# Performance work log

Measured on AMD Instinct MI355X. Metric: run time of the kernel, lower is better.

The kernel has to match this reference:

```python
import jax, jax.numpy as jnp
import numpy as np

B, L, H, E, D = 4, 2048, 8, 64, 64  # seq S == L (causal mask requires square scores)


def setup_inputs() -> dict:
    key = jax.random.key(0)
    k0, k1, k2, k3, k4 = jax.random.split(key, 5)
    queries = jax.random.normal(k0, (B, L, H, E), jnp.float32)
    keys = jax.random.normal(k1, (B, L, H, E), jnp.float32)
    values = jax.random.normal(k2, (B, L, H, D), jnp.float32)
    # per-sample learned de-stationary scale (positive) and bias
    tau = jax.random.uniform(k3, (B, 1, 1), jnp.float32, 0.5, 1.5)
    delta = jax.random.normal(k4, (B, 1, L), jnp.float32) * 0.1
    return {"queries": queries, "keys": keys, "values": values, "tau": tau, "delta": delta}


def reference(queries, keys, values, tau, delta):
    Bq, Lq, Hq, Eq = queries.shape
    S = keys.shape[1]
    scale = 1.0 / jnp.sqrt(jnp.asarray(Eq, jnp.float32))
    # torch path: rearrange('b s h d l -> (b d) s h l') with s=h=d=1 -> [B,1,1,1] / [B,1,1,S]
    tau_b = tau.reshape(Bq, 1, 1, 1)
    delta_b = delta.reshape(Bq, 1, 1, -1)[..., :S]
    # scores: [B, H, L, S]
    scores = jnp.einsum('blhe,bshe->bhls', queries, keys) * tau_b + delta_b
    causal = jnp.triu(jnp.ones((Lq, S), bool), k=1)  # True above diagonal -> masked
    scores = jnp.where(causal, -jnp.inf, scores)
    A = jax.nn.softmax(scale * scores, axis=-1)  # dropout is identity in eval/reference
    V = jnp.einsum('bhls,bshd->blhd', A, values)  # [B, L, H, D]
    return V
```

## Files before the change

kernel.cpp:

```cpp
#include <hip/hip_runtime.h>
#include <hip/hip_bf16.h>

#define Bsz 4
#define Lsz 2048
#define Hsz 8

typedef __attribute__((ext_vector_type(8)))  short bf16x8;
typedef __attribute__((ext_vector_type(4)))  short bf16x4;
typedef __attribute__((ext_vector_type(4)))  float f32x4;

__device__ __forceinline__ short f2bs(float f) {
    union { float f; unsigned u; } v; v.f = f;
    unsigned r = v.u + 0x7FFFu + ((v.u >> 16) & 1u);
    return (short)(r >> 16);
}
__device__ __forceinline__ short f2bs_rh(float f) {
    return (short)((__float_as_uint(f) + 0x8000u) >> 16);
}

__device__ __forceinline__ void stage16(const short* g, short* l) {
    __builtin_amdgcn_global_load_lds(
        (const __attribute__((address_space(1))) unsigned int*)g,
        (__attribute__((address_space(3))) unsigned int*)l,
        16, 0, 0);
}

__global__ __launch_bounds__(256) void prep_kv(
    const float* __restrict__ ksrc, const float* __restrict__ vsrc,
    const float* __restrict__ delta,
    short* __restrict__ Kf, short* __restrict__ Vf, float* __restrict__ Df)
{
    const int raw = blockIdx.x;
    const int tid = threadIdx.x;
    if (raw >= 2*Bsz*Hsz*32) {
        const float c2 = 0.125f * 1.44269504f;
        const int base = ((raw - 2*Bsz*Hsz*32)*256 + tid) * 16;
        #pragma unroll
        for (int u = 0; u < 4; ++u) {
            float4 v = *(const float4*)(delta + base + u*4);
            v.x*=c2; v.y*=c2; v.z*=c2; v.w*=c2;
            *(float4*)(Df + base + u*4) = v;
        }
        return;
    }
    __shared__ float Tl[64][65];
    const bool isK = raw < Bsz*Hsz*32;
    const int bid = isK ? raw : raw - Bsz*Hsz*32;
    const int tl = bid & 31, bh = bid >> 5;
    const int b = bh >> 3, h = bh & 7;

    const int row = tid >> 2, c0 = (tid & 3) * 16;
    const float* src = (isK ? ksrc : vsrc)
                     + (((size_t)b*Lsz + tl*64 + row)*Hsz + h)*64 + c0;
    *(float4*)&Tl[row][c0]      = *(const float4*)(src);
    *(float4*)&Tl[row][c0 + 4]  = *(const float4*)(src + 4);
    *(float4*)&Tl[row][c0 + 8]  = *(const float4*)(src + 8);
    *(float4*)&Tl[row][c0 + 12] = *(const float4*)(src + 12);
    __syncthreads();

    const int lane = tid & 63, ln = lane & 15, quad = lane >> 4;
    if (isK) {
        short* dst = Kf + (size_t)bid * 4096;
        #pragma unroll
        for (int cc = 0; cc < 2; ++cc) {
            const int c  = (tid >> 6)*2 + cc;
            const int kq = c >> 1, eb = c & 1;
            const float* rp = &Tl[kq*16 + ln][eb*32 + quad*8];
            bf16x8 o = {f2bs(rp[0]),f2bs(rp[1]),f2bs(rp[2]),f2bs(rp[3]),
                        f2bs(rp[4]),f2bs(rp[5]),f2bs(rp[6]),f2bs(rp[7])};
            *(bf16x8*)(dst + c*512 + lane*8) = o;
        }
    } else {
        short* dst = Vf + (size_t)bid * 4096;
        #pragma unroll
        for (int cc = 0; cc < 2; ++cc) {
            const int c   = (tid >> 6)*2 + cc;
            const int kq  = c >> 1, dgp = c & 1;
            const int s0  = kq*16 + quad*4;
            const int d0  = dgp*32 + ln;
            const int d1  = dgp*32 + 16 + ln;
            bf16x8 o = {f2bs(Tl[s0+0][d0]), f2bs(Tl[s0+1][d0]),
                        f2bs(Tl[s0+2][d0]), f2bs(Tl[s0+3][d0]),
                        f2bs(Tl[s0+0][d1]), f2bs(Tl[s0+1][d1]),
                        f2bs(Tl[s0+2][d1]), f2bs(Tl[s0+3][d1])};
            *(bf16x8*)(dst + c*512 + lane*8) = o;
        }
    }
}

__global__ __launch_bounds__(256, 4) void dsattn_main(
    const float* __restrict__ q,
    const short* __restrict__ Kf,
    const short* __restrict__ Vf,
    const float* __restrict__ Df,
    const float* __restrict__ tau,
    float* __restrict__ out)
{
    __shared__ __align__(16) short Kb[2][4096];
    __shared__ __align__(16) short Vb[2][4096];
    __shared__ __align__(16) short Qs[4096];

    const int tid  = threadIdx.x;
    const int kq   = tid >> 6;
    const int lane = tid & 63;
    const int ln   = lane & 15;
    const int quad = lane >> 4;

    const int bh = blockIdx.x;
    const int b  = bh >> 3, h = bh & 7;
    const int y = blockIdx.y, g8 = y >> 3, a = y & 7;
    const int qt = (g8 == 0) ? 31 - 2*a : (g8 == 1) ? 2*a
                 : (g8 == 2) ? 30 - 2*a : 2*a + 1;
    const int q0 = qt * 64;
    const int T  = qt + 1;

    const float st2 = (0.125f * 1.44269504f) * tau[b];

    const short* gK = Kf + (size_t)bh*(32*4096) + kq*1024 + lane*8;
    const short* gV = Vf + (size_t)bh*(32*4096) + kq*1024 + lane*8;
    const float* Dfp = Df + (size_t)b*Lsz + kq*16 + quad*4;

    short* const myK0 = &Kb[0][kq*1024];
    short* const myV0 = &Vb[0][kq*1024];

#define STAGE(buf) do {                                                     \
        short* k_ = (buf) ? myK0 + 4096 : myK0;                             \
        short* v_ = (buf) ? myV0 + 4096 : myV0;                             \
        stage16(gK + 0*512, k_ + 0*512);                                    \
        stage16(gK + 1*512, k_ + 1*512);                                    \
        stage16(gV + 0*512, v_ + 0*512);                                    \
        stage16(gV + 1*512, v_ + 1*512);                                    \
        gK += 4096; gV += 4096;                                             \
        __builtin_amdgcn_sched_barrier(0);                                  \
    } while (0)
#define WAITN(n) do {                                                       \
        asm volatile("s_waitcnt vmcnt(" #n ")" ::: "memory");               \
        __builtin_amdgcn_sched_barrier(0);                                  \
    } while (0)

    STAGE(0);
    f32x4 dlv_c = *(const f32x4*)(Dfp); Dfp += 64;

    {
        const float* qrow = q + (((size_t)b*Lsz + q0 + kq*16 + ln)*Hsz + h)*64;
        float4 a0 = *(const float4*)(qrow + quad*8);
        float4 a1 = *(const float4*)(qrow + quad*8 + 4);
        float4 b0 = *(const float4*)(qrow + 32 + quad*8);
        float4 b1 = *(const float4*)(qrow + 32 + quad*8 + 4);
        bf16x8 q0f = {f2bs(a0.x),f2bs(a0.y),f2bs(a0.z),f2bs(a0.w),
                      f2bs(a1.x),f2bs(a1.y),f2bs(a1.z),f2bs(a1.w)};
        bf16x8 q1f = {f2bs(b0.x),f2bs(b0.y),f2bs(b0.z),f2bs(b0.w),
                      f2bs(b1.x),f2bs(b1.y),f2bs(b1.z),f2bs(b1.w)};
        *(bf16x8*)(&Qs[(kq*2+0)*512 + lane*8]) = q0f;
        *(bf16x8*)(&Qs[(kq*2+1)*512 + lane*8]) = q1f;
    }

    f32x4 oacc[4][4];
    #pragma unroll
    for (int dg = 0; dg < 4; ++dg)
        #pragma unroll
        for (int qg = 0; qg < 4; ++qg)
            oacc[dg][qg] = (f32x4){0.f,0.f,0.f,0.f};
    float l_acc[4] = {0.f,0.f,0.f,0.f};

    __syncthreads();

#define TILE_BODY(t_, MASKED, HASNEXT) do {                                 \
        const short* Kc_ = ((t_) & 1) ? myK0 + 4096 : myK0;                 \
        const short* Vc_ = ((t_) & 1) ? myV0 + 4096 : myV0;                 \
        f32x4 dlv_n_;                                                       \
        if (HASNEXT) {                                                      \
            STAGE(((t_)+1) & 1);                                            \
            dlv_n_ = *(const f32x4*)(Dfp); Dfp += 64;                       \
        }                                                                   \
        if (HASNEXT) WAITN(8); else WAITN(3);            \
        bf16x8 kf0_ = *(const bf16x8*)(Kc_ + 0*512 + lane*8);               \
        bf16x8 kf1_ = *(const bf16x8*)(Kc_ + 1*512 + lane*8);               \
        f32x4 sacc_[4];                                                     \
        __builtin_amdgcn_s_setprio(1);                                      \
        _Pragma("unroll")                                                   \
        for (int qg = 0; qg < 4; ++qg) {                                    \
            bf16x8 qa_ = *(const bf16x8*)(&Qs[(qg*2+0)*512 + lane*8]);      \
            bf16x8 qb_ = *(const bf16x8*)(&Qs[(qg*2+1)*512 + lane*8]);      \
            f32x4 z_ = (f32x4){0.f,0.f,0.f,0.f};                            \
            z_ = __builtin_amdgcn_mfma_f32_16x16x32_bf16(kf0_, qa_, z_, 0,0,0); \
            sacc_[qg] = __builtin_amdgcn_mfma_f32_16x16x32_bf16(kf1_, qb_, z_, 0,0,0); \
        }                                                                   \
        __builtin_amdgcn_s_setprio(0);                                      \
        if (MASKED) {                                                       \
            _Pragma("unroll")                                               \
            for (int qg = 0; qg < 4; ++qg)                                  \
                _Pragma("unroll")                                           \
                for (int r = 0; r < 4; ++r)                                 \
                    if (kq*16 + quad*4 + r > qg*16 + ln) sacc_[qg][r] = -1e30f; \
        }                                                                   \
        bf16x4 pT_[4];                                                      \
        _Pragma("unroll")                                                   \
        for (int qg = 0; qg < 4; ++qg) {                                    \
            float p0_ = __builtin_amdgcn_exp2f(fmaf(sacc_[qg][0], st2, dlv_c[0])); \
            float p1_ = __builtin_amdgcn_exp2f(fmaf(sacc_[qg][1], st2, dlv_c[1])); \
            float p2_ = __builtin_amdgcn_exp2f(fmaf(sacc_[qg][2], st2, dlv_c[2])); \
            float p3_ = __builtin_amdgcn_exp2f(fmaf(sacc_[qg][3], st2, dlv_c[3])); \
            l_acc[qg] += (p0_ + p1_) + (p2_ + p3_);                         \
            pT_[qg] = (bf16x4){f2bs_rh(p0_), f2bs_rh(p1_),                  \
                               f2bs_rh(p2_), f2bs_rh(p3_)};                 \
        }                                                                   \
        if (HASNEXT) dlv_c = dlv_n_;                                        \
        if (HASNEXT) WAITN(5); else WAITN(0);         \
        bf16x4 vf_[4];                                                      \
        _Pragma("unroll")                                                   \
        for (int dg = 0; dg < 4; ++dg)                                      \
            vf_[dg] = *(const bf16x4*)(Vc_ + (dg>>1)*512 + lane*8 + (dg&1)*4); \
        __builtin_amdgcn_s_setprio(1);                                      \
        _Pragma("unroll")                                                   \
        for (int dg = 0; dg < 4; ++dg)                                      \
            _Pragma("unroll")                                               \
            for (int qg = 0; qg < 4; ++qg)                                  \
                oacc[dg][qg] = __builtin_amdgcn_mfma_f32_16x16x16bf16_1k(   \
                    vf_[dg], pT_[qg], oacc[dg][qg], 0,0,0);                 \
        __builtin_amdgcn_s_setprio(0);                                      \
    } while (0)

    for (int t = 0; t < T - 1; ++t) TILE_BODY(t, false, true);
    TILE_BODY(T - 1, true, false);

    float lq[4];
    #pragma unroll
    for (int qg = 0; qg < 4; ++qg) {
        float s = l_acc[qg];
        s += __shfl_xor(s, 16, 64);
        s += __shfl_xor(s, 32, 64);
        lq[qg] = s;
    }
    float* KbF = (float*)&Kb[0][0];
    float* VbF = (float*)&Vb[0][0];
    float* lred = (float*)&Qs[0];
    __syncthreads();

    if (lane < 16)
        #pragma unroll
        for (int qg = 0; qg < 4; ++qg) lred[kq*64 + qg*16 + ln] = lq[qg];
    if (kq == 1 || kq == 3) {
        float* dst = (kq == 1) ? KbF : VbF;
        #pragma unroll
        for (int dg = 0; dg < 4; ++dg)
            #pragma unroll
            for (int qg = 0; qg < 4; ++qg)
                *(f32x4*)(dst + (dg*4+qg)*256 + lane*4) = oacc[dg][qg];
    }
    __syncthreads();
    if (kq == 0 || kq == 2) {
        const float* srcp = (kq == 0) ? KbF : VbF;
        #pragma unroll
        for (int dg = 0; dg < 4; ++dg)
            #pragma unroll
            for (int qg = 0; qg < 4; ++qg) {
                f32x4 v = *(const f32x4*)(srcp + (dg*4+qg)*256 + lane*4);
                oacc[dg][qg][0] += v[0]; oacc[dg][qg][1] += v[1];
                oacc[dg][qg][2] += v[2]; oacc[dg][qg][3] += v[3];
            }
    }
    __syncthreads();
    if (kq == 2) {
        #pragma unroll
        for (int dg = 0; dg < 4; ++dg)
            #pragma unroll
            for (int qg = 0; qg < 4; ++qg)
                *(f32x4*)(KbF + (dg*4+qg)*256 + lane*4) = oacc[dg][qg];
    }
    __syncthreads();
    if (kq == 0) {
        float inv[4];
        #pragma unroll
        for (int qg = 0; qg < 4; ++qg)
            inv[qg] = 1.0f / (lred[qg*16 + ln] + lred[64 + qg*16 + ln]
                            + lred[128 + qg*16 + ln] + lred[192 + qg*16 + ln]);
        #pragma unroll
        for (int qg = 0; qg < 4; ++qg) {
            float* orow = out + (((size_t)b*Lsz + q0 + qg*16 + ln)*Hsz + h)*64;
            #pragma unroll
            for (int dg = 0; dg < 4; ++dg) {
                f32x4 v = *(const f32x4*)(KbF + (dg*4+qg)*256 + lane*4);
                float4 o = {(oacc[dg][qg][0] + v[0]) * inv[qg],
                            (oacc[dg][qg][1] + v[1]) * inv[qg],
                            (oacc[dg][qg][2] + v[2]) * inv[qg],
                            (oacc[dg][qg][3] + v[3]) * inv[qg]};
                *(float4*)(orow + dg*16 + quad*4) = o;
            }
        }
    }
#undef STAGE
#undef WAITN
#undef TILE_BODY
}

extern "C" void kernel_launch(void* const* d_in, const int* in_sizes, int n_in,
                              void* d_out, int out_size, void* d_ws, size_t ws_size,
                              hipStream_t stream) {
    (void)in_sizes; (void)n_in; (void)out_size; (void)ws_size;
    const float* q     = (const float*)d_in[0];
    const float* k     = (const float*)d_in[1];
    const float* v     = (const float*)d_in[2];
    const float* tau   = (const float*)d_in[3];
    const float* delta = (const float*)d_in[4];
    float* out = (float*)d_out;

    short* Kf = (short*)d_ws;
    short* Vf = (short*)d_ws + (size_t)(4*1024*1024);
    float* Df = (float*)((char*)d_ws + (size_t)(16*1024*1024));

    prep_kv<<<dim3(Bsz*Hsz*32*2 + 2), dim3(256), 0, stream>>>(k, v, delta, Kf, Vf, Df);
    dsattn_main<<<dim3(Bsz*Hsz, 32), dim3(256), 0, stream>>>(q, Kf, Vf, Df, tau, out);
}
```

Baseline: 129.6 us.

## Keep Q fragments in registers and stage scaled delta row in LDS

The delta prescale pass is removed from the prep kernel. Each attention block now loads its batch's delta row once, scales it and stores it in LDS, so the per-tile global delta load and its vmcnt accounting go away. Q is converted into per-wave register fragments for all four query groups instead of going through shared memory, and V is read with two 16-byte LDS loads instead of four 8-byte loads. This raises register pressure and relies on a syncthreads later in the kernel before the delta LDS reads, while freeing LDS traffic and global loads in the inner loop.

```diff
diff --git a/kernel.cpp b/kernel.cpp
--- a/kernel.cpp
+++ b/kernel.cpp
@@ -27,23 +27,11 @@
 
 __global__ __launch_bounds__(256) void prep_kv(
     const float* __restrict__ ksrc, const float* __restrict__ vsrc,
-    const float* __restrict__ delta,
-    short* __restrict__ Kf, short* __restrict__ Vf, float* __restrict__ Df)
+    short* __restrict__ Kf, short* __restrict__ Vf)
 {
+    __shared__ float Tl[64][65];
     const int raw = blockIdx.x;
     const int tid = threadIdx.x;
-    if (raw >= 2*Bsz*Hsz*32) {
-        const float c2 = 0.125f * 1.44269504f;
-        const int base = ((raw - 2*Bsz*Hsz*32)*256 + tid) * 16;
-        #pragma unroll
-        for (int u = 0; u < 4; ++u) {
-            float4 v = *(const float4*)(delta + base + u*4);
-            v.x*=c2; v.y*=c2; v.z*=c2; v.w*=c2;
-            *(float4*)(Df + base + u*4) = v;
-        }
-        return;
-    }
-    __shared__ float Tl[64][65];
     const bool isK = raw < Bsz*Hsz*32;
     const int bid = isK ? raw : raw - Bsz*Hsz*32;
     const int tl = bid & 31, bh = bid >> 5;
@@ -92,13 +80,13 @@
     const float* __restrict__ q,
     const short* __restrict__ Kf,
     const short* __restrict__ Vf,
-    const float* __restrict__ Df,
     const float* __restrict__ tau,
+    const float* __restrict__ delta,
     float* __restrict__ out)
 {
     __shared__ __align__(16) short Kb[2][4096];
     __shared__ __align__(16) short Vb[2][4096];
-    __shared__ __align__(16) short Qs[4096];
+    __shared__ float dls[Lsz];
 
     const int tid  = threadIdx.x;
     const int kq   = tid >> 6;
@@ -114,11 +102,11 @@
     const int q0 = qt * 64;
     const int T  = qt + 1;
 
-    const float st2 = (0.125f * 1.44269504f) * tau[b];
+    const float c2  = 0.125f * 1.44269504f;
+    const float st2 = c2 * tau[b];
 
     const short* gK = Kf + (size_t)bh*(32*4096) + kq*1024 + lane*8;
     const short* gV = Vf + (size_t)bh*(32*4096) + kq*1024 + lane*8;
-    const float* Dfp = Df + (size_t)b*Lsz + kq*16 + quad*4;
 
     short* const myK0 = &Kb[0][kq*1024];
     short* const myV0 = &Vb[0][kq*1024];
@@ -139,20 +127,29 @@
     } while (0)
 
     STAGE(0);
-    f32x4 dlv_c = *(const f32x4*)(Dfp); Dfp += 64;
 
     {
-        const float* qrow = q + (((size_t)b*Lsz + q0 + kq*16 + ln)*Hsz + h)*64;
+        const float* dsrc = delta + (size_t)b*Lsz + tid*8;
+        float4 av = *(const float4*)(dsrc);
+        float4 cv = *(const float4*)(dsrc + 4);
+        av.x*=c2; av.y*=c2; av.z*=c2; av.w*=c2;
+        cv.x*=c2; cv.y*=c2; cv.z*=c2; cv.w*=c2;
+        *(float4*)&dls[tid*8]     = av;
+        *(float4*)&dls[tid*8 + 4] = cv;
+    }
+
+    bf16x8 qf[4][2];
+    #pragma unroll
+    for (int qg = 0; qg < 4; ++qg) {
+        const float* qrow = q + (((size_t)b*Lsz + q0 + qg*16 + ln)*Hsz + h)*64;
         float4 a0 = *(const float4*)(qrow + quad*8);
         float4 a1 = *(const float4*)(qrow + quad*8 + 4);
         float4 b0 = *(const float4*)(qrow + 32 + quad*8);
         float4 b1 = *(const float4*)(qrow + 32 + quad*8 + 4);
-        bf16x8 q0f = {f2bs(a0.x),f2bs(a0.y),f2bs(a0.z),f2bs(a0.w),
-                      f2bs(a1.x),f2bs(a1.y),f2bs(a1.z),f2bs(a1.w)};
-        bf16x8 q1f = {f2bs(b0.x),f2bs(b0.y),f2bs(b0.z),f2bs(b0.w),
-                      f2bs(b1.x),f2bs(b1.y),f2bs(b1.z),f2bs(b1.w)};
-        *(bf16x8*)(&Qs[(kq*2+0)*512 + lane*8]) = q0f;
-        *(bf16x8*)(&Qs[(kq*2+1)*512 + lane*8]) = q1f;
+        qf[qg][0] = (bf16x8){f2bs(a0.x),f2bs(a0.y),f2bs(a0.z),f2bs(a0.w),
+                             f2bs(a1.x),f2bs(a1.y),f2bs(a1.z),f2bs(a1.w)};
+        qf[qg][1] = (bf16x8){f2bs(b0.x),f2bs(b0.y),f2bs(b0.z),f2bs(b0.w),
+                             f2bs(b1.x),f2bs(b1.y),f2bs(b1.z),f2bs(b1.w)};
     }
 
     f32x4 oacc[4][4];
@@ -168,23 +165,17 @@
 #define TILE_BODY(t_, MASKED, HASNEXT) do {                                 \
         const short* Kc_ = ((t_) & 1) ? myK0 + 4096 : myK0;                 \
         const short* Vc_ = ((t_) & 1) ? myV0 + 4096 : myV0;                 \
-        f32x4 dlv_n_;                                                       \
-        if (HASNEXT) {                                                      \
-            STAGE(((t_)+1) & 1);                                            \
-            dlv_n_ = *(const f32x4*)(Dfp); Dfp += 64;                       \
-        }                                                                   \
-        if (HASNEXT) WAITN(8); else WAITN(3);            \
+        if (HASNEXT) STAGE(((t_)+1) & 1);                                   \
+        if (HASNEXT) WAITN(6); else WAITN(2);            \
         bf16x8 kf0_ = *(const bf16x8*)(Kc_ + 0*512 + lane*8);               \
         bf16x8 kf1_ = *(const bf16x8*)(Kc_ + 1*512 + lane*8);               \
         f32x4 sacc_[4];                                                     \
         __builtin_amdgcn_s_setprio(1);                                      \
         _Pragma("unroll")                                                   \
         for (int qg = 0; qg < 4; ++qg) {                                    \
-            bf16x8 qa_ = *(const bf16x8*)(&Qs[(qg*2+0)*512 + lane*8]);      \
-            bf16x8 qb_ = *(const bf16x8*)(&Qs[(qg*2+1)*512 + lane*8]);      \
             f32x4 z_ = (f32x4){0.f,0.f,0.f,0.f};                            \
-            z_ = __builtin_amdgcn_mfma_f32_16x16x32_bf16(kf0_, qa_, z_, 0,0,0); \
-            sacc_[qg] = __builtin_amdgcn_mfma_f32_16x16x32_bf16(kf1_, qb_, z_, 0,0,0); \
+            z_ = __builtin_amdgcn_mfma_f32_16x16x32_bf16(kf0_, qf[qg][0], z_, 0,0,0); \
+            sacc_[qg] = __builtin_amdgcn_mfma_f32_16x16x32_bf16(kf1_, qf[qg][1], z_, 0,0,0); \
         }                                                                   \
         __builtin_amdgcn_s_setprio(0);                                      \
         if (MASKED) {                                                       \
@@ -194,23 +185,26 @@
                 for (int r = 0; r < 4; ++r)                                 \
                     if (kq*16 + quad*4 + r > qg*16 + ln) sacc_[qg][r] = -1e30f; \
         }                                                                   \
+        f32x4 dlv_ = *(const f32x4*)&dls[(t_)*64 + kq*16 + quad*4];         \
         bf16x4 pT_[4];                                                      \
         _Pragma("unroll")                                                   \
         for (int qg = 0; qg < 4; ++qg) {                                    \
-            float p0_ = __builtin_amdgcn_exp2f(fmaf(sacc_[qg][0], st2, dlv_c[0])); \
-            float p1_ = __builtin_amdgcn_exp2f(fmaf(sacc_[qg][1], st2, dlv_c[1])); \
-            float p2_ = __builtin_amdgcn_exp2f(fmaf(sacc_[qg][2], st2, dlv_c[2])); \
-            float p3_ = __builtin_amdgcn_exp2f(fmaf(sacc_[qg][3], st2, dlv_c[3])); \
+            float p0_ = __builtin_amdgcn_exp2f(fmaf(sacc_[qg][0], st2, dlv_[0])); \
+            float p1_ = __builtin_amdgcn_exp2f(fmaf(sacc_[qg][1], st2, dlv_[1])); \
+            float p2_ = __builtin_amdgcn_exp2f(fmaf(sacc_[qg][2], st2, dlv_[2])); \
+            float p3_ = __builtin_amdgcn_exp2f(fmaf(sacc_[qg][3], st2, dlv_[3])); \
             l_acc[qg] += (p0_ + p1_) + (p2_ + p3_);                         \
             pT_[qg] = (bf16x4){f2bs_rh(p0_), f2bs_rh(p1_),                  \
                                f2bs_rh(p2_), f2bs_rh(p3_)};                 \
         }                                                                   \
-        if (HASNEXT) dlv_c = dlv_n_;                                        \
-        if (HASNEXT) WAITN(5); else WAITN(0);         \
+        if (HASNEXT) WAITN(4); else WAITN(0);            \
+        bf16x8 vv0_ = *(const bf16x8*)(Vc_ + 0*512 + lane*8);               \
+        bf16x8 vv1_ = *(const bf16x8*)(Vc_ + 1*512 + lane*8);               \
         bf16x4 vf_[4];                                                      \
-        _Pragma("unroll")                                                   \
-        for (int dg = 0; dg < 4; ++dg)                                      \
-            vf_[dg] = *(const bf16x4*)(Vc_ + (dg>>1)*512 + lane*8 + (dg&1)*4); \
+        vf_[0] = (bf16x4){vv0_[0], vv0_[1], vv0_[2], vv0_[3]};              \
+        vf_[1] = (bf16x4){vv0_[4], vv0_[5], vv0_[6], vv0_[7]};              \
+        vf_[2] = (bf16x4){vv1_[0], vv1_[1], vv1_[2], vv1_[3]};              \
+        vf_[3] = (bf16x4){vv1_[4], vv1_[5], vv1_[6], vv1_[7]};              \
         __builtin_amdgcn_s_setprio(1);                                      \
         _Pragma("unroll")                                                   \
         for (int dg = 0; dg < 4; ++dg)                                      \
@@ -234,7 +228,7 @@
     }
     float* KbF = (float*)&Kb[0][0];
     float* VbF = (float*)&Vb[0][0];
-    float* lred = (float*)&Qs[0];
+    float* lred = dls;
     __syncthreads();
 
     if (lane < 16)
@@ -307,8 +301,7 @@
 
     short* Kf = (short*)d_ws;
     short* Vf = (short*)d_ws + (size_t)(4*1024*1024);
-    float* Df = (float*)((char*)d_ws + (size_t)(16*1024*1024));
-
-    prep_kv<<<dim3(Bsz*Hsz*32*2 + 2), dim3(256), 0, stream>>>(k, v, delta, Kf, Vf, Df);
-    dsattn_main<<<dim3(Bsz*Hsz, 32), dim3(256), 0, stream>>>(q, Kf, Vf, Df, tau, out);
-}
+
+    prep_kv<<<dim3(Bsz*Hsz*32*2), dim3(256), 0, stream>>>(k, v, Kf, Vf);
+    dsattn_main<<<dim3(Bsz*Hsz, 32), dim3(256), 0, stream>>>(q, Kf, Vf, tau, delta, out);
+}
```

Measured after the change: 155.5 us. 20.0% more time.
